# Optimization experiments

Hardware: AMD Instinct MI355X
Metric: run time of the kernel (lower is better)

## Reference

```python
import jax, jax.numpy as jnp
import numpy as np

nT, nB, nC = 128, 256, 512      # encoder timesteps, batch, feature channels (= input_size)
H = 512                          # hidden_size
L = 26                           # decode steps per sample (uniform text_length)
NCLS = 6736                      # num_classes


def setup_inputs() -> dict:
    key = jax.random.key(0)
    ks = jax.random.split(key, 12)
    g = lambda k, shp, s: (jax.random.normal(k, shp, jnp.float32) * s)
    return {
        "feats": jax.random.normal(ks[0], (nT, nB, nC), jnp.float32),
        "text_length": jnp.full((nB,), L, dtype=jnp.int32),
        # AttentionCell params (torch Linear weight layout: [out, in])
        "W_i2h": g(ks[1], (H, nC), 0.04),          # i2h, no bias
        "W_h2h": g(ks[2], (H, H), 0.04),
        "b_h2h": g(ks[3], (H,), 0.04),
        "W_score": g(ks[4], (1, H), 0.04),          # score, no bias
        # GRUCell params, gate order r,z,n
        "W_ih": g(ks[5], (3 * H, nC), 0.04),
        "W_hh": g(ks[6], (3 * H, H), 0.04),
        "b_ih": g(ks[7], (3 * H,), 0.04),
        "b_hh": g(ks[8], (3 * H,), 0.04),
        # generator
        "W_gen": g(ks[9], (NCLS, H), 0.04),
        "b_gen": g(ks[10], (NCLS,), 0.04),
    }


def reference(feats, text_length, W_i2h, W_h2h, b_h2h, W_score, W_ih, W_hh,
              b_ih, b_hh, W_gen, b_gen):
    T, B, C = feats.shape
    steps = int(np.asarray(text_length).max())  # uniform lengths -> static loop count

    # i2h(feats) does not depend on the hidden state: precompute once.
    feats_proj = jnp.einsum('tbc,hc->tbh', feats, W_i2h)  # [T,B,H]
    w_score = W_score[0]                                   # [H]

    def step(h, _):
        # Bahdanau attention (original runs per-sample with nB==1; batched here)
        hp = h @ W_h2h.T + b_h2h                           # [B,H]
        e = jnp.einsum('tbh,h->tb', jnp.tanh(feats_proj + hp[None]), w_score)
        alpha = jax.nn.softmax(e, axis=0)                  # softmax over T (nB==1 case)
        context = jnp.einsum('tb,tbc->bc', alpha, feats)   # [B,C]
        # GRUCell(context, h), torch gate order r,z,n
        gi = context @ W_ih.T + b_ih                       # [B,3H]
        gh = h @ W_hh.T + b_hh                             # [B,3H]
        ir, iz, i_n = jnp.split(gi, 3, axis=1)
        hr, hz, h_n = jnp.split(gh, 3, axis=1)
        r = jax.nn.sigmoid(ir + hr)
        z = jax.nn.sigmoid(iz + hz)
        n = jnp.tanh(i_n + r * h_n)
        h_new = (1.0 - z) * n + z * h
        return h_new, h_new

    h0 = jnp.zeros((B, W_h2h.shape[0]), feats.dtype)
    _, hs = jax.lax.scan(step, h0, None, length=steps)     # [steps,B,H]

    # original fills output_hiddens with k = j*L + i ordering (batch outer, step inner)
    out_h = hs.transpose(1, 0, 2).reshape(B * steps, -1)   # [num_labels,H]
    probs = out_h @ W_gen.T + b_gen                        # [num_labels,NCLS]
    return probs
```

## Files before the change

kernel.cpp:

```cpp
#include <hip/hip_runtime.h>

#define T_   128
#define B_   256
#define C_   512
#define H_   512
#define L_   26
#define NCLS 6736
#define NPAD 6784

typedef __attribute__((ext_vector_type(8))) short short8;
typedef __attribute__((ext_vector_type(4))) float f32x4;

__device__ __forceinline__ unsigned short f2b(float f) {
    union { float f; unsigned int u; } v; v.f = f;
    unsigned int r = (v.u + 0x7fffu + ((v.u >> 16) & 1u)) >> 16;
    return (unsigned short)r;
}
__device__ __forceinline__ float b2f(unsigned short u) {
    union { unsigned int u; float f; } v; v.u = ((unsigned int)u) << 16;
    return v.f;
}
__device__ __forceinline__ float tanh_fast(float x) {
    float e = __expf(2.f * x);
    return 1.f - 2.f / (e + 1.f);
}
__device__ __forceinline__ float sigm(float x) {
    return 1.f / (1.f + __expf(-x));
}
__device__ __forceinline__ void llds16(const unsigned short* g, unsigned short* l) {
    __builtin_amdgcn_global_load_lds(
        (const __attribute__((address_space(1))) void*)g,
        (__attribute__((address_space(3))) void*)l, 16, 0, 0);
}

__global__ __launch_bounds__(256) void prep_kernel(
    const float* __restrict__ feats, const float* __restrict__ W_i2h,
    const float* __restrict__ W_gen, const float* __restrict__ W_h2h,
    const float* __restrict__ W_hh, const float* __restrict__ W_ih,
    unsigned short* __restrict__ feats16, unsigned short* __restrict__ wi2h16,
    unsigned short* __restrict__ wgen16, unsigned short* __restrict__ w2hT16,
    unsigned short* __restrict__ whh16, unsigned short* __restrict__ wih16,
    float* __restrict__ h32, unsigned short* __restrict__ h16)
{
    size_t idx = (size_t)blockIdx.x * 256 + threadIdx.x;
    feats16[idx] = f2b(feats[idx]);
    if (idx < (size_t)H_ * C_) wi2h16[idx] = f2b(W_i2h[idx]);
    if (idx < (size_t)NPAD * H_)
        wgen16[idx] = (idx < (size_t)NCLS * H_) ? f2b(W_gen[idx]) : (unsigned short)0;
    if (idx < (size_t)H_ * H_)
        w2hT16[idx] = f2b(W_h2h[(idx & 511) * 512 + (idx >> 9)]);
    if (idx < (size_t)1536 * 512) {
        whh16[idx] = f2b(W_hh[idx]);
        wih16[idx] = f2b(W_ih[idx]);
    }
    if (idx < (size_t)B_ * H_) { h32[idx] = 0.f; h16[idx] = 0; }
}

template<int OUTMODE>
__global__ __launch_bounds__(256) void gemm_bt(
    const unsigned short* __restrict__ A, const unsigned short* __restrict__ B,
    void* __restrict__ outp, const float* __restrict__ bias,
    int M, int N, int K, int ncols)
{
    __shared__ unsigned short As[128 * 32];
    __shared__ unsigned short Bs[128 * 32];
    const int tid = threadIdx.x;
    const int lane = tid & 63;

    const int gridN = (int)gridDim.x, gridM = (int)gridDim.y;
    const int bid = (int)blockIdx.y * gridN + (int)blockIdx.x;
    const int GM = 8;
    const int per = GM * gridN;
    const int grp = bid / per;
    const int rem = bid - grp * per;
    const int gsz0 = gridM - grp * GM;
    const int gsz = gsz0 < GM ? gsz0 : GM;
    const int m0 = (grp * GM + rem % gsz) * 128;
    const int n0 = (rem / gsz) * 128;

    const int wv = tid >> 6;
    const int wm = (wv >> 1) * 64;
    const int wn = (wv & 1) * 64;

    f32x4 acc[4][4];
#pragma unroll
    for (int i = 0; i < 4; i++)
#pragma unroll
        for (int j = 0; j < 4; j++) acc[i][j] = (f32x4)0.f;

    for (int k0 = 0; k0 < K; k0 += 32) {
        __syncthreads();
#pragma unroll
        for (int is = 0; is < 2; ++is) {
            int c = is * 256 + tid;
            int row = c >> 2, col = (c & 3) * 8;
            llds16(A + (size_t)(m0 + row) * K + k0 + col, &As[c * 8]);
            llds16(B + (size_t)(n0 + row) * K + k0 + col, &Bs[c * 8]);
        }
        __syncthreads();
        short8 af[4], bf[4];
#pragma unroll
        for (int t = 0; t < 4; t++) {
            af[t] = *(const short8*)&As[(wm + t * 16 + (lane & 15)) * 32 + (lane >> 4) * 8];
            bf[t] = *(const short8*)&Bs[(wn + t * 16 + (lane & 15)) * 32 + (lane >> 4) * 8];
        }
#pragma unroll
        for (int i = 0; i < 4; i++)
#pragma unroll
            for (int j = 0; j < 4; j++)
                acc[i][j] = __builtin_amdgcn_mfma_f32_16x16x32_bf16(af[i], bf[j], acc[i][j], 0, 0, 0);
    }

    const int cr = (lane >> 4) * 4;
    const int cc = lane & 15;
    if constexpr (OUTMODE == 0) {
        unsigned short* o = (unsigned short*)outp;
#pragma unroll
        for (int i = 0; i < 4; i++)
#pragma unroll
            for (int j = 0; j < 4; j++) {
                int col = n0 + wn + j * 16 + cc;
#pragma unroll
                for (int r = 0; r < 4; r++) {
                    int row = m0 + wm + i * 16 + cr + r;
                    o[(size_t)row * N + col] = f2b(acc[i][j][r]);
                }
            }
    } else {
        float* o = (float*)outp;
#pragma unroll
        for (int j = 0; j < 4; j++) {
            int col = n0 + wn + j * 16 + cc;
            if (col < ncols) {
                float bv = bias[col];
#pragma unroll
                for (int i = 0; i < 4; i++)
#pragma unroll
                    for (int r = 0; r < 4; r++) {
                        int row = m0 + wm + i * 16 + cr + r;
                        o[(size_t)row * ncols + col] = acc[i][j][r] + bv;
                    }
            }
        }
    }
}

__global__ __launch_bounds__(1024) void attn_mega(
    const unsigned short* __restrict__ fp, const unsigned short* __restrict__ feats16,
    const unsigned short* __restrict__ h16, const unsigned short* __restrict__ w2hT,
    const float* __restrict__ b_h2h, const float* __restrict__ wscore,
    unsigned short* __restrict__ ctx16)
{
    const int b = blockIdx.x;
    const int tid = threadIdx.x, lane = tid & 63, wv = tid >> 6;
    __shared__ float se[T_];
    __shared__ float ctx4[4][C_];
    __shared__ float shp[H_];
    __shared__ float shh[H_];

    if (tid < H_) shh[tid] = b2f(h16[(size_t)b * H_ + tid]);
    __syncthreads();

    {
        const int col = tid & (H_ - 1);
        const int kh = tid >> 9;
        const unsigned short* wp = w2hT + (size_t)(kh << 8) * H_ + col;
        const float* hh = &shh[kh << 8];
        float a0 = 0.f, a1 = 0.f;
#pragma unroll 8
        for (int k = 0; k < 256; k += 2) {
            a0 += hh[k]     * b2f(wp[(size_t)k * H_]);
            a1 += hh[k + 1] * b2f(wp[(size_t)(k + 1) * H_]);
        }
        ctx4[kh][col] = a0 + a1;
    }
    __syncthreads();
    if (tid < H_) shp[tid] = ctx4[0][tid] + ctx4[1][tid] + b_h2h[tid];
    __syncthreads();

    float hpr[8], wsr[8];
    {
        const float* wb = wscore + lane * 8;
        const float* hb = &shp[lane * 8];
#pragma unroll
        for (int i = 0; i < 8; i++) { hpr[i] = hb[i]; wsr[i] = wb[i]; }
    }
#pragma unroll
    for (int i = 0; i < 8; i++) {
        int t = wv * 8 + i;
        short8 v = *(const short8*)(fp + ((size_t)t * B_ + b) * H_ + lane * 8);
        float p = 0.f;
#pragma unroll
        for (int j = 0; j < 8; j++)
            p += wsr[j] * tanh_fast(b2f((unsigned short)v[j]) + hpr[j]);
#pragma unroll
        for (int off = 32; off > 0; off >>= 1) p += __shfl_xor(p, off, 64);
        if (lane == 0) se[t] = p;
    }
    __syncthreads();
    if (wv == 0) {
        float v0 = se[lane], v1 = se[lane + 64];
        float mx = fmaxf(v0, v1);
#pragma unroll
        for (int off = 32; off > 0; off >>= 1) mx = fmaxf(mx, __shfl_xor(mx, off, 64));
        float e0 = __expf(v0 - mx), e1 = __expf(v1 - mx);
        float s = e0 + e1;
#pragma unroll
        for (int off = 32; off > 0; off >>= 1) s += __shfl_xor(s, off, 64);
        float inv = 1.f / s;
        se[lane] = e0 * inv; se[lane + 64] = e1 * inv;
    }
    __syncthreads();
    const int c = (tid & 255) * 2;
    const int q = tid >> 8;
    float a0 = 0.f, a1 = 0.f;
    const unsigned short* fb = feats16 + (size_t)b * C_ + c;
    for (int i = 0; i < 32; i++) {
        int t = q * 32 + i;
        float al = se[t];
        unsigned int u = *(const unsigned int*)(fb + (size_t)t * B_ * C_);
        a0 += al * b2f((unsigned short)(u & 0xffffu));
        a1 += al * b2f((unsigned short)(u >> 16));
    }
    ctx4[q][c] = a0; ctx4[q][c + 1] = a1;
    __syncthreads();
    if (tid < C_) {
        float s = ctx4[0][tid] + ctx4[1][tid] + ctx4[2][tid] + ctx4[3][tid];
        ctx16[(size_t)b * C_ + tid] = f2b(s);
    }
}

__global__ __launch_bounds__(256) void gates_mega(
    const unsigned short* __restrict__ ctx, const unsigned short* __restrict__ wih,
    const unsigned short* __restrict__ hin16, const unsigned short* __restrict__ whh,
    const float* __restrict__ b_ih, const float* __restrict__ b_hh,
    const float* __restrict__ hin32, float* __restrict__ hout32,
    unsigned short* __restrict__ hout16, unsigned short* __restrict__ outH, int step)
{
    const int tid = threadIdx.x, lane = tid & 63, wv = tid >> 6;
    const int m0 = blockIdx.y * 16;
    const int n0 = blockIdx.x * 64 + wv * 16;
    const unsigned short* ap = ctx   + (size_t)(m0 + (lane & 15)) * C_ + (lane >> 4) * 8;
    const unsigned short* ah = hin16 + (size_t)(m0 + (lane & 15)) * H_ + (lane >> 4) * 8;
    const unsigned short* bp = wih + (size_t)(n0 + (lane & 15)) * H_ + (lane >> 4) * 8;
    const unsigned short* bh = whh + (size_t)(n0 + (lane & 15)) * H_ + (lane >> 4) * 8;
    f32x4 ar = (f32x4)0.f, az = (f32x4)0.f, an = (f32x4)0.f;
    f32x4 gr = (f32x4)0.f, gz = (f32x4)0.f, gn = (f32x4)0.f;
#pragma unroll
    for (int k0 = 0; k0 < H_; k0 += 32) {
        short8 a  = *(const short8*)(ap + k0);
        short8 a2 = *(const short8*)(ah + k0);
        short8 br = *(const short8*)(bp + k0);
        short8 bz = *(const short8*)(bp + (size_t)512 * H_ + k0);
        short8 bn = *(const short8*)(bp + (size_t)1024 * H_ + k0);
        short8 cr_ = *(const short8*)(bh + k0);
        short8 cz_ = *(const short8*)(bh + (size_t)512 * H_ + k0);
        short8 cn_ = *(const short8*)(bh + (size_t)1024 * H_ + k0);
        ar = __builtin_amdgcn_mfma_f32_16x16x32_bf16(a,  br,  ar, 0, 0, 0);
        az = __builtin_amdgcn_mfma_f32_16x16x32_bf16(a,  bz,  az, 0, 0, 0);
        an = __builtin_amdgcn_mfma_f32_16x16x32_bf16(a,  bn,  an, 0, 0, 0);
        gr = __builtin_amdgcn_mfma_f32_16x16x32_bf16(a2, cr_, gr, 0, 0, 0);
        gz = __builtin_amdgcn_mfma_f32_16x16x32_bf16(a2, cz_, gz, 0, 0, 0);
        gn = __builtin_amdgcn_mfma_f32_16x16x32_bf16(a2, cn_, gn, 0, 0, 0);
    }
    const int cc = lane & 15, cr = (lane >> 4) * 4;
    const int col = n0 + cc;
    const float bir = b_ih[col], biz = b_ih[512 + col], bin = b_ih[1024 + col];
    const float bhr = b_hh[col], bhz = b_hh[512 + col], bhn = b_hh[1024 + col];
#pragma unroll
    for (int r = 0; r < 4; r++) {
        int row = m0 + cr + r;
        float hv = hin32[(size_t)row * H_ + col];
        float rg = sigm(ar[r] + bir + gr[r] + bhr);
        float zg = sigm(az[r] + biz + gz[r] + bhz);
        float ng = tanh_fast(an[r] + bin + rg * (gn[r] + bhn));
        float hn = (1.f - zg) * ng + zg * hv;
        hout32[(size_t)row * H_ + col] = hn;
        unsigned short hb = f2b(hn);
        hout16[(size_t)row * H_ + col] = hb;
        outH[((size_t)row * L_ + step) * H_ + col] = hb;
    }
}

extern "C" void kernel_launch(void* const* d_in, const int* in_sizes, int n_in,
                              void* d_out, int out_size, void* d_ws, size_t ws_size,
                              hipStream_t stream)
{
    const float* feats   = (const float*)d_in[0];
    const float* W_i2h   = (const float*)d_in[2];
    const float* W_h2h   = (const float*)d_in[3];
    const float* b_h2h   = (const float*)d_in[4];
    const float* W_score = (const float*)d_in[5];
    const float* W_ih    = (const float*)d_in[6];
    const float* W_hh    = (const float*)d_in[7];
    const float* b_ih    = (const float*)d_in[8];
    const float* b_hh    = (const float*)d_in[9];
    const float* W_gen   = (const float*)d_in[10];
    const float* b_gen   = (const float*)d_in[11];

    char* ws = (char*)d_ws;
    size_t off = 0;
    auto alloc = [&](size_t bytes) {
        void* p = ws + off; off += (bytes + 255) & ~(size_t)255; return p;
    };
    unsigned short* feats16 = (unsigned short*)alloc((size_t)T_ * B_ * C_ * 2);
    unsigned short* fp16    = (unsigned short*)alloc((size_t)T_ * B_ * H_ * 2);
    unsigned short* wgen16  = (unsigned short*)alloc((size_t)NPAD * H_ * 2);
    unsigned short* wi2h16  = (unsigned short*)alloc((size_t)H_ * C_ * 2);
    unsigned short* w2hT16  = (unsigned short*)alloc((size_t)H_ * H_ * 2);
    unsigned short* whh16   = (unsigned short*)alloc((size_t)1536 * 512 * 2);
    unsigned short* wih16   = (unsigned short*)alloc((size_t)1536 * 512 * 2);
    unsigned short* outH16  = (unsigned short*)alloc((size_t)B_ * L_ * H_ * 2);
    float* h32a = (float*)alloc((size_t)B_ * H_ * 4);
    float* h32b = (float*)alloc((size_t)B_ * H_ * 4);
    unsigned short* h16a = (unsigned short*)alloc((size_t)B_ * H_ * 2);
    unsigned short* h16b = (unsigned short*)alloc((size_t)B_ * H_ * 2);
    unsigned short* ctx16 = (unsigned short*)alloc((size_t)B_ * C_ * 2);

    prep_kernel<<<dim3((T_ * B_ * C_) / 256), 256, 0, stream>>>(
        feats, W_i2h, W_gen, W_h2h, W_hh, W_ih,
        feats16, wi2h16, wgen16, w2hT16, whh16, wih16, h32a, h16a);

    gemm_bt<0><<<dim3(H_ / 128, (T_ * B_) / 128), 256, 0, stream>>>(
        feats16, wi2h16, fp16, nullptr, T_ * B_, H_, C_, 0);

    for (int s = 0; s < L_; s++) {
        const float* hin32          = (s & 1) ? h32b : h32a;
        float* hout32               = (s & 1) ? h32a : h32b;
        const unsigned short* hin16 = (s & 1) ? h16b : h16a;
        unsigned short* hout16      = (s & 1) ? h16a : h16b;
        attn_mega<<<dim3(B_), 1024, 0, stream>>>(
            fp16, feats16, hin16, w2hT16, b_h2h, W_score, ctx16);
        gates_mega<<<dim3(8, 16), 256, 0, stream>>>(
            ctx16, wih16, hin16, whh16, b_ih, b_hh, hin32, hout32, hout16, outH16, s);
    }

    gemm_bt<1><<<dim3(NPAD / 128, (B_ * L_) / 128), 256, 0, stream>>>(
        outH16, wgen16, d_out, b_gen, B_ * L_, NPAD, H_, NCLS);
}
```

Before: 1.516 ms.

## Fuse recurrent loop into persistent kernel with software grid barriers

Replaces the 52 per-step kernel launches (attention and GRU gates) with one persistent kernel of 256 blocks that loops over all decode steps and synchronises through a flag-based grid barrier. The h2h projection becomes a separate MFMA phase writing hp to global memory, and the GRU gates phase is spread over 512 waves. The aim is to remove launch overhead and tail effects between the many small kernels. In exchange it adds three grid barriers per step, and the barrier has a spin cap that could break out early and silently produce wrong results if blocks are not co-resident.

After: 4.051 ms. 2.67x slower.

```diff
diff --git a/kernel.cpp b/kernel.cpp
--- a/kernel.cpp
+++ b/kernel.cpp
@@ -7,6 +7,8 @@
 #define L_   26
 #define NCLS 6736
 #define NPAD 6784
+#define GRID_P 256
+#define BAR_CAP 65536
 
 typedef __attribute__((ext_vector_type(8))) short short8;
 typedef __attribute__((ext_vector_type(4))) float f32x4;
@@ -31,6 +33,37 @@
     __builtin_amdgcn_global_load_lds(
         (const __attribute__((address_space(1))) void*)g,
         (__attribute__((address_space(3))) void*)l, 16, 0, 0);
+}
+
+__device__ __forceinline__ void gridbar(unsigned* flags, unsigned* gen, unsigned ep) {
+    __syncthreads();
+    if (blockIdx.x == 0) {
+        const int t = threadIdx.x;
+        if (t > 0 && t < GRID_P) {
+            int it = 0;
+            while (__hip_atomic_load(&flags[t * 16], __ATOMIC_ACQUIRE,
+                                     __HIP_MEMORY_SCOPE_AGENT) < ep) {
+                if (++it > BAR_CAP) break;
+                __builtin_amdgcn_s_sleep(8);
+            }
+        }
+        __syncthreads();
+        if (t == 0)
+            __hip_atomic_store(gen, ep, __ATOMIC_RELEASE, __HIP_MEMORY_SCOPE_AGENT);
+        __syncthreads();
+    } else {
+        if (threadIdx.x == 0) {
+            __hip_atomic_store(&flags[blockIdx.x * 16], ep, __ATOMIC_RELEASE,
+                               __HIP_MEMORY_SCOPE_AGENT);
+            int it = 0;
+            while (__hip_atomic_load(gen, __ATOMIC_ACQUIRE,
+                                     __HIP_MEMORY_SCOPE_AGENT) < ep) {
+                if (++it > BAR_CAP) break;
+                __builtin_amdgcn_s_sleep(8);
+            }
+        }
+        __syncthreads();
+    }
 }
 
 __global__ __launch_bounds__(256) void prep_kernel(
@@ -38,22 +71,21 @@
     const float* __restrict__ W_gen, const float* __restrict__ W_h2h,
     const float* __restrict__ W_hh, const float* __restrict__ W_ih,
     unsigned short* __restrict__ feats16, unsigned short* __restrict__ wi2h16,
-    unsigned short* __restrict__ wgen16, unsigned short* __restrict__ w2hT16,
-    unsigned short* __restrict__ whh16, unsigned short* __restrict__ wih16,
-    float* __restrict__ h32, unsigned short* __restrict__ h16)
+    unsigned short* __restrict__ wgen16, unsigned short* __restrict__ w1_16,
+    unsigned short* __restrict__ wih16,
+    float* __restrict__ h32, unsigned short* __restrict__ h16,
+    unsigned* __restrict__ bar)
 {
     size_t idx = (size_t)blockIdx.x * 256 + threadIdx.x;
     feats16[idx] = f2b(feats[idx]);
     if (idx < (size_t)H_ * C_) wi2h16[idx] = f2b(W_i2h[idx]);
     if (idx < (size_t)NPAD * H_)
         wgen16[idx] = (idx < (size_t)NCLS * H_) ? f2b(W_gen[idx]) : (unsigned short)0;
-    if (idx < (size_t)H_ * H_)
-        w2hT16[idx] = f2b(W_h2h[(idx & 511) * 512 + (idx >> 9)]);
-    if (idx < (size_t)1536 * 512) {
-        whh16[idx] = f2b(W_hh[idx]);
-        wih16[idx] = f2b(W_ih[idx]);
-    }
+    if (idx < (size_t)2048 * 512)
+        w1_16[idx] = f2b(idx < 262144 ? W_h2h[idx] : W_hh[idx - 262144]);
+    if (idx < (size_t)1536 * 512) wih16[idx] = f2b(W_ih[idx]);
     if (idx < (size_t)B_ * H_) { h32[idx] = 0.f; h16[idx] = 0; }
+    if (idx < 4160) bar[idx] = 0u;
 }
 
 template<int OUTMODE>
@@ -145,140 +177,148 @@
     }
 }
 
-__global__ __launch_bounds__(1024) void attn_mega(
+__global__ __launch_bounds__(512, 2) void recurrent_persist(
     const unsigned short* __restrict__ fp, const unsigned short* __restrict__ feats16,
-    const unsigned short* __restrict__ h16, const unsigned short* __restrict__ w2hT,
-    const float* __restrict__ b_h2h, const float* __restrict__ wscore,
-    unsigned short* __restrict__ ctx16)
+    const unsigned short* __restrict__ w1, const unsigned short* __restrict__ wih,
+    const float* __restrict__ b_h2h, const float* __restrict__ b_hh,
+    const float* __restrict__ b_ih, const float* __restrict__ wscore,
+    float* __restrict__ h32a, float* __restrict__ h32b,
+    unsigned short* __restrict__ h16a, unsigned short* __restrict__ h16b,
+    float* __restrict__ hp, unsigned short* __restrict__ ctx16,
+    unsigned short* __restrict__ outH,
+    unsigned* __restrict__ flags, unsigned* __restrict__ gen)
 {
     const int b = blockIdx.x;
     const int tid = threadIdx.x, lane = tid & 63, wv = tid >> 6;
+    const int u = wv * GRID_P + b;
     __shared__ float se[T_];
-    __shared__ float ctx4[4][C_];
-    __shared__ float shp[H_];
-    __shared__ float shh[H_];
-
-    if (tid < H_) shh[tid] = b2f(h16[(size_t)b * H_ + tid]);
-    __syncthreads();
-
-    {
-        const int col = tid & (H_ - 1);
-        const int kh = tid >> 9;
-        const unsigned short* wp = w2hT + (size_t)(kh << 8) * H_ + col;
-        const float* hh = &shh[kh << 8];
-        float a0 = 0.f, a1 = 0.f;
-#pragma unroll 8
-        for (int k = 0; k < 256; k += 2) {
-            a0 += hh[k]     * b2f(wp[(size_t)k * H_]);
-            a1 += hh[k + 1] * b2f(wp[(size_t)(k + 1) * H_]);
-        }
-        ctx4[kh][col] = a0 + a1;
-    }
-    __syncthreads();
-    if (tid < H_) shp[tid] = ctx4[0][tid] + ctx4[1][tid] + b_h2h[tid];
-    __syncthreads();
-
-    float hpr[8], wsr[8];
-    {
-        const float* wb = wscore + lane * 8;
-        const float* hb = &shp[lane * 8];
-#pragma unroll
-        for (int i = 0; i < 8; i++) { hpr[i] = hb[i]; wsr[i] = wb[i]; }
-    }
-#pragma unroll
-    for (int i = 0; i < 8; i++) {
-        int t = wv * 8 + i;
-        short8 v = *(const short8*)(fp + ((size_t)t * B_ + b) * H_ + lane * 8);
-        float p = 0.f;
-#pragma unroll
-        for (int j = 0; j < 8; j++)
-            p += wsr[j] * tanh_fast(b2f((unsigned short)v[j]) + hpr[j]);
-#pragma unroll
-        for (int off = 32; off > 0; off >>= 1) p += __shfl_xor(p, off, 64);
-        if (lane == 0) se[t] = p;
-    }
-    __syncthreads();
-    if (wv == 0) {
-        float v0 = se[lane], v1 = se[lane + 64];
-        float mx = fmaxf(v0, v1);
-#pragma unroll
-        for (int off = 32; off > 0; off >>= 1) mx = fmaxf(mx, __shfl_xor(mx, off, 64));
-        float e0 = __expf(v0 - mx), e1 = __expf(v1 - mx);
-        float s = e0 + e1;
-#pragma unroll
-        for (int off = 32; off > 0; off >>= 1) s += __shfl_xor(s, off, 64);
-        float inv = 1.f / s;
-        se[lane] = e0 * inv; se[lane + 64] = e1 * inv;
-    }
-    __syncthreads();
-    const int c = (tid & 255) * 2;
-    const int q = tid >> 8;
-    float a0 = 0.f, a1 = 0.f;
-    const unsigned short* fb = feats16 + (size_t)b * C_ + c;
-    for (int i = 0; i < 32; i++) {
-        int t = q * 32 + i;
-        float al = se[t];
-        unsigned int u = *(const unsigned int*)(fb + (size_t)t * B_ * C_);
-        a0 += al * b2f((unsigned short)(u & 0xffffu));
-        a1 += al * b2f((unsigned short)(u >> 16));
-    }
-    ctx4[q][c] = a0; ctx4[q][c + 1] = a1;
-    __syncthreads();
-    if (tid < C_) {
-        float s = ctx4[0][tid] + ctx4[1][tid] + ctx4[2][tid] + ctx4[3][tid];
-        ctx16[(size_t)b * C_ + tid] = f2b(s);
-    }
-}
-
-__global__ __launch_bounds__(256) void gates_mega(
-    const unsigned short* __restrict__ ctx, const unsigned short* __restrict__ wih,
-    const unsigned short* __restrict__ hin16, const unsigned short* __restrict__ whh,
-    const float* __restrict__ b_ih, const float* __restrict__ b_hh,
-    const float* __restrict__ hin32, float* __restrict__ hout32,
-    unsigned short* __restrict__ hout16, unsigned short* __restrict__ outH, int step)
-{
-    const int tid = threadIdx.x, lane = tid & 63, wv = tid >> 6;
-    const int m0 = blockIdx.y * 16;
-    const int n0 = blockIdx.x * 64 + wv * 16;
-    const unsigned short* ap = ctx   + (size_t)(m0 + (lane & 15)) * C_ + (lane >> 4) * 8;
-    const unsigned short* ah = hin16 + (size_t)(m0 + (lane & 15)) * H_ + (lane >> 4) * 8;
-    const unsigned short* bp = wih + (size_t)(n0 + (lane & 15)) * H_ + (lane >> 4) * 8;
-    const unsigned short* bh = whh + (size_t)(n0 + (lane & 15)) * H_ + (lane >> 4) * 8;
-    f32x4 ar = (f32x4)0.f, az = (f32x4)0.f, an = (f32x4)0.f;
-    f32x4 gr = (f32x4)0.f, gz = (f32x4)0.f, gn = (f32x4)0.f;
-#pragma unroll
-    for (int k0 = 0; k0 < H_; k0 += 32) {
-        short8 a  = *(const short8*)(ap + k0);
-        short8 a2 = *(const short8*)(ah + k0);
-        short8 br = *(const short8*)(bp + k0);
-        short8 bz = *(const short8*)(bp + (size_t)512 * H_ + k0);
-        short8 bn = *(const short8*)(bp + (size_t)1024 * H_ + k0);
-        short8 cr_ = *(const short8*)(bh + k0);
-        short8 cz_ = *(const short8*)(bh + (size_t)512 * H_ + k0);
-        short8 cn_ = *(const short8*)(bh + (size_t)1024 * H_ + k0);
-        ar = __builtin_amdgcn_mfma_f32_16x16x32_bf16(a,  br,  ar, 0, 0, 0);
-        az = __builtin_amdgcn_mfma_f32_16x16x32_bf16(a,  bz,  az, 0, 0, 0);
-        an = __builtin_amdgcn_mfma_f32_16x16x32_bf16(a,  bn,  an, 0, 0, 0);
-        gr = __builtin_amdgcn_mfma_f32_16x16x32_bf16(a2, cr_, gr, 0, 0, 0);
-        gz = __builtin_amdgcn_mfma_f32_16x16x32_bf16(a2, cz_, gz, 0, 0, 0);
-        gn = __builtin_amdgcn_mfma_f32_16x16x32_bf16(a2, cn_, gn, 0, 0, 0);
-    }
-    const int cc = lane & 15, cr = (lane >> 4) * 4;
-    const int col = n0 + cc;
-    const float bir = b_ih[col], biz = b_ih[512 + col], bin = b_ih[1024 + col];
-    const float bhr = b_hh[col], bhz = b_hh[512 + col], bhn = b_hh[1024 + col];
-#pragma unroll
-    for (int r = 0; r < 4; r++) {
-        int row = m0 + cr + r;
-        float hv = hin32[(size_t)row * H_ + col];
-        float rg = sigm(ar[r] + bir + gr[r] + bhr);
-        float zg = sigm(az[r] + biz + gz[r] + bhz);
-        float ng = tanh_fast(an[r] + bin + rg * (gn[r] + bhn));
-        float hn = (1.f - zg) * ng + zg * hv;
-        hout32[(size_t)row * H_ + col] = hn;
-        unsigned short hb = f2b(hn);
-        hout16[(size_t)row * H_ + col] = hb;
-        outH[((size_t)row * L_ + step) * H_ + col] = hb;
+    __shared__ float ctx4[2][C_];
+    unsigned ep = 0;
+
+    for (int s = 0; s < L_; ++s) {
+        const float* hin32          = (s & 1) ? h32b : h32a;
+        float* hout32               = (s & 1) ? h32a : h32b;
+        const unsigned short* hin16 = (s & 1) ? h16b : h16a;
+        unsigned short* hout16      = (s & 1) ? h16a : h16b;
+
+        if (u < 512) {
+            const int m0 = (u >> 5) * 16;
+            const int n0 = (u & 31) * 16;
+            const unsigned short* ap = hin16 + (size_t)(m0 + (lane & 15)) * H_ + (lane >> 4) * 8;
+            const unsigned short* bp = w1 + (size_t)(n0 + (lane & 15)) * H_ + (lane >> 4) * 8;
+            f32x4 acc = (f32x4)0.f;
+#pragma unroll
+            for (int k0 = 0; k0 < H_; k0 += 32) {
+                short8 a  = *(const short8*)(ap + k0);
+                short8 b0 = *(const short8*)(bp + k0);
+                acc = __builtin_amdgcn_mfma_f32_16x16x32_bf16(a, b0, acc, 0, 0, 0);
+            }
+            const int cc = lane & 15, cr = (lane >> 4) * 4;
+            const int col = n0 + cc;
+            const float bv = b_h2h[col];
+#pragma unroll
+            for (int r = 0; r < 4; r++)
+                hp[(size_t)(m0 + cr + r) * H_ + col] = acc[r] + bv;
+        }
+        ++ep; gridbar(flags, gen, ep);
+
+        {
+            float hpr[8], wsr[8];
+            {
+                const float* hb = hp + b * H_ + lane * 8;
+                const float* wb = wscore + lane * 8;
+#pragma unroll
+                for (int i = 0; i < 8; i++) { hpr[i] = hb[i]; wsr[i] = wb[i]; }
+            }
+#pragma unroll
+            for (int i = 0; i < 16; i++) {
+                int t = wv * 16 + i;
+                short8 v = *(const short8*)(fp + ((size_t)t * B_ + b) * H_ + lane * 8);
+                float p = 0.f;
+#pragma unroll
+                for (int j = 0; j < 8; j++)
+                    p += wsr[j] * tanh_fast(b2f((unsigned short)v[j]) + hpr[j]);
+#pragma unroll
+                for (int off = 32; off > 0; off >>= 1) p += __shfl_xor(p, off, 64);
+                if (lane == 0) se[t] = p;
+            }
+            __syncthreads();
+            if (wv == 0) {
+                float v0 = se[lane], v1 = se[lane + 64];
+                float mx = fmaxf(v0, v1);
+#pragma unroll
+                for (int off = 32; off > 0; off >>= 1) mx = fmaxf(mx, __shfl_xor(mx, off, 64));
+                float e0 = __expf(v0 - mx), e1 = __expf(v1 - mx);
+                float sm = e0 + e1;
+#pragma unroll
+                for (int off = 32; off > 0; off >>= 1) sm += __shfl_xor(sm, off, 64);
+                float inv = 1.f / sm;
+                se[lane] = e0 * inv; se[lane + 64] = e1 * inv;
+            }
+            __syncthreads();
+            const int c = (tid & 255) * 2;
+            const int q = tid >> 8;
+            float a0 = 0.f, a1 = 0.f;
+            const unsigned short* fb = feats16 + (size_t)b * C_ + c;
+            for (int i = 0; i < 64; i++) {
+                int t = q * 64 + i;
+                float al = se[t];
+                unsigned int uu = *(const unsigned int*)(fb + (size_t)t * B_ * C_);
+                a0 += al * b2f((unsigned short)(uu & 0xffffu));
+                a1 += al * b2f((unsigned short)(uu >> 16));
+            }
+            ctx4[q][c] = a0; ctx4[q][c + 1] = a1;
+            __syncthreads();
+            float sc = ctx4[0][tid] + ctx4[1][tid];
+            ctx16[(size_t)b * C_ + tid] = f2b(sc);
+        }
+        ++ep; gridbar(flags, gen, ep);
+
+        if (u < 512) {
+            const int m0 = (u >> 5) * 16;
+            const int n0 = (u & 31) * 16;
+            const unsigned short* ap = ctx16 + (size_t)(m0 + (lane & 15)) * C_ + (lane >> 4) * 8;
+            const unsigned short* ah = hin16 + (size_t)(m0 + (lane & 15)) * H_ + (lane >> 4) * 8;
+            const unsigned short* bp = wih + (size_t)(n0 + (lane & 15)) * H_ + (lane >> 4) * 8;
+            const unsigned short* bh = w1 + 262144 + (size_t)(n0 + (lane & 15)) * H_ + (lane >> 4) * 8;
+            f32x4 ar = (f32x4)0.f, az = (f32x4)0.f, an = (f32x4)0.f;
+            f32x4 gr = (f32x4)0.f, gz = (f32x4)0.f, gn = (f32x4)0.f;
+#pragma unroll
+            for (int k0 = 0; k0 < H_; k0 += 32) {
+                short8 a   = *(const short8*)(ap + k0);
+                short8 a2  = *(const short8*)(ah + k0);
+                short8 br  = *(const short8*)(bp + k0);
+                short8 bz  = *(const short8*)(bp + (size_t)512 * H_ + k0);
+                short8 bn  = *(const short8*)(bp + (size_t)1024 * H_ + k0);
+                short8 cr_ = *(const short8*)(bh + k0);
+                short8 cz_ = *(const short8*)(bh + (size_t)512 * H_ + k0);
+                short8 cn_ = *(const short8*)(bh + (size_t)1024 * H_ + k0);
+                ar = __builtin_amdgcn_mfma_f32_16x16x32_bf16(a,  br,  ar, 0, 0, 0);
+                az = __builtin_amdgcn_mfma_f32_16x16x32_bf16(a,  bz,  az, 0, 0, 0);
+                an = __builtin_amdgcn_mfma_f32_16x16x32_bf16(a,  bn,  an, 0, 0, 0);
+                gr = __builtin_amdgcn_mfma_f32_16x16x32_bf16(a2, cr_, gr, 0, 0, 0);
+                gz = __builtin_amdgcn_mfma_f32_16x16x32_bf16(a2, cz_, gz, 0, 0, 0);
+                gn = __builtin_amdgcn_mfma_f32_16x16x32_bf16(a2, cn_, gn, 0, 0, 0);
+            }
+            const int cc = lane & 15, cr = (lane >> 4) * 4;
+            const int col = n0 + cc;
+            const float bir = b_ih[col], biz = b_ih[512 + col], bin = b_ih[1024 + col];
+            const float bhr = b_hh[col], bhz = b_hh[512 + col], bhn = b_hh[1024 + col];
+#pragma unroll
+            for (int r = 0; r < 4; r++) {
+                int row = m0 + cr + r;
+                float hv = hin32[(size_t)row * H_ + col];
+                float rg = sigm(ar[r] + bir + gr[r] + bhr);
+                float zg = sigm(az[r] + biz + gz[r] + bhz);
+                float ng = tanh_fast(an[r] + bin + rg * (gn[r] + bhn));
+                float hn = (1.f - zg) * ng + zg * hv;
+                hout32[(size_t)row * H_ + col] = hn;
+                unsigned short hb = f2b(hn);
+                hout16[(size_t)row * H_ + col] = hb;
+                outH[((size_t)row * L_ + s) * H_ + col] = hb;
+            }
+        }
+        ++ep; gridbar(flags, gen, ep);
     }
 }
 
@@ -307,33 +347,27 @@
     unsigned short* fp16    = (unsigned short*)alloc((size_t)T_ * B_ * H_ * 2);
     unsigned short* wgen16  = (unsigned short*)alloc((size_t)NPAD * H_ * 2);
     unsigned short* wi2h16  = (unsigned short*)alloc((size_t)H_ * C_ * 2);
-    unsigned short* w2hT16  = (unsigned short*)alloc((size_t)H_ * H_ * 2);
-    unsigned short* whh16   = (unsigned short*)alloc((size_t)1536 * 512 * 2);
+    unsigned short* w1_16   = (unsigned short*)alloc((size_t)2048 * 512 * 2);
     unsigned short* wih16   = (unsigned short*)alloc((size_t)1536 * 512 * 2);
     unsigned short* outH16  = (unsigned short*)alloc((size_t)B_ * L_ * H_ * 2);
     float* h32a = (float*)alloc((size_t)B_ * H_ * 4);
     float* h32b = (float*)alloc((size_t)B_ * H_ * 4);
     unsigned short* h16a = (unsigned short*)alloc((size_t)B_ * H_ * 2);
     unsigned short* h16b = (unsigned short*)alloc((size_t)B_ * H_ * 2);
+    float* hp_buf = (float*)alloc((size_t)B_ * H_ * 4);
     unsigned short* ctx16 = (unsigned short*)alloc((size_t)B_ * C_ * 2);
+    unsigned* bar = (unsigned*)alloc(4160 * 4);
 
     prep_kernel<<<dim3((T_ * B_ * C_) / 256), 256, 0, stream>>>(
         feats, W_i2h, W_gen, W_h2h, W_hh, W_ih,
-        feats16, wi2h16, wgen16, w2hT16, whh16, wih16, h32a, h16a);
+        feats16, wi2h16, wgen16, w1_16, wih16, h32a, h16a, bar);
 
     gemm_bt<0><<<dim3(H_ / 128, (T_ * B_) / 128), 256, 0, stream>>>(
         feats16, wi2h16, fp16, nullptr, T_ * B_, H_, C_, 0);
 
-    for (int s = 0; s < L_; s++) {
-        const float* hin32          = (s & 1) ? h32b : h32a;
-        float* hout32               = (s & 1) ? h32a : h32b;
-        const unsigned short* hin16 = (s & 1) ? h16b : h16a;
-        unsigned short* hout16      = (s & 1) ? h16a : h16b;
-        attn_mega<<<dim3(B_), 1024, 0, stream>>>(
-            fp16, feats16, hin16, w2hT16, b_h2h, W_score, ctx16);
-        gates_mega<<<dim3(8, 16), 256, 0, stream>>>(
-            ctx16, wih16, hin16, whh16, b_ih, b_hh, hin32, hout32, hout16, outH16, s);
-    }
+    recurrent_persist<<<dim3(GRID_P), 512, 0, stream>>>(
+        fp16, feats16, w1_16, wih16, b_h2h, b_hh, b_ih, W_score,
+        h32a, h32b, h16a, h16b, hp_buf, ctx16, outH16, bar, bar + 4096);
 
     gemm_bt<1><<<dim3(NPAD / 128, (B_ * L_) / 128), 256, 0, stream>>>(
         outH16, wgen16, d_out, b_gen, B_ * L_, NPAD, H_, NCLS);
```
